# Optimization experiments

Measured on AMD Instinct MI355X. Metric: run time of the kernel, lower is better.

## Reference

```python
import jax, jax.numpy as jnp
import numpy as np

N_NODES = 100000


def _gcn_norm(src, dst, n_nodes, n_edges):
    # PyG gcn_norm with add_self_loops=False: deg over target (col) index
    ones = jnp.ones((n_edges,), dtype=jnp.float32)
    deg = jax.ops.segment_sum(ones, dst, num_segments=n_nodes)
    dinv = jnp.where(deg > 0, jax.lax.rsqrt(deg), 0.0)
    return dinv[src] * dinv[dst]  # [E]


def _arma_conv(x, src, dst, ew, init_w, root_w, bias, n_nodes):
    # x: [N, Fin]; init_w/root_w: [K, Fin, Fout]; bias: [K, 1, Fout]
    h = jnp.einsum('nf,kfo->kno', x, init_w)          # [K, N, Fout]
    msg = h[:, src, :] * ew[None, :, None]             # [K, E, Fout]
    agg = jax.vmap(lambda m: jax.ops.segment_sum(m, dst, num_segments=n_nodes))(msg)
    out = agg + jnp.einsum('nf,kfo->kno', x, root_w) + bias
    return jax.nn.relu(out).mean(axis=0)               # mean over stacks K


def setup_inputs() -> dict:
    key = jax.random.key(0)
    ks = jax.random.split(key, 8)
    n, e = N_NODES, 3200000
    nfeat, hid, nclass, K = 512, 16, 40, 2
    x = jax.random.normal(ks[0], (n, nfeat), dtype=jnp.float32)
    edge_index = jax.random.randint(ks[1], (2, e), 0, n, dtype=jnp.int32)
    s1 = (1.0 / np.sqrt(nfeat)).astype(np.float32) if isinstance(np.sqrt(nfeat), np.ndarray) else np.float32(1.0 / np.sqrt(nfeat))
    s2 = np.float32(1.0 / np.sqrt(hid))
    iw1 = jax.random.normal(ks[2], (K, nfeat, hid), dtype=jnp.float32) * s1
    rw1 = jax.random.normal(ks[3], (K, nfeat, hid), dtype=jnp.float32) * s1
    b1 = jax.random.normal(ks[4], (K, 1, hid), dtype=jnp.float32) * 0.01
    iw2 = jax.random.normal(ks[5], (K, hid, nclass), dtype=jnp.float32) * s2
    rw2 = jax.random.normal(ks[6], (K, hid, nclass), dtype=jnp.float32) * s2
    b2 = jax.random.normal(ks[7], (K, 1, nclass), dtype=jnp.float32) * 0.01
    return {'x': x, 'edge_index': edge_index, 'iw1': iw1, 'rw1': rw1, 'b1': b1,
            'iw2': iw2, 'rw2': rw2, 'b2': b2}


def reference(x, edge_index, iw1, rw1, b1, iw2, rw2, b2):
    src, dst = edge_index[0], edge_index[1]
    n = N_NODES
    ew = _gcn_norm(src, dst, n, src.shape[0])
    h = _arma_conv(x, src, dst, ew, iw1, rw1, b1, n)   # [N, 16]
    out = _arma_conv(h, src, dst, ew, iw2, rw2, b2, n) # [N, nclass]
    return out
```

## Files before the change

kernel.cpp:

```cpp
#include <hip/hip_runtime.h>


#define TB 256
#define CHA 4096

typedef __attribute__((ext_vector_type(8))) short bf8;
typedef __attribute__((ext_vector_type(4))) float f4;

__device__ inline unsigned short f2bf_rne(float f) {
  unsigned int u = __float_as_uint(f);
  unsigned int r = u + 0x7fffu + ((u >> 16) & 1u);
  return (unsigned short)(r >> 16);
}
__device__ inline float bf2f(unsigned short h) {
  return __uint_as_float(((unsigned int)h) << 16);
}
__device__ inline float bflo(unsigned int u) { return __uint_as_float(u << 16); }
__device__ inline float bfhi(unsigned int u) { return __uint_as_float(u & 0xffff0000u); }
__device__ inline unsigned int bfpack(float lo, float hi) {
  return (unsigned int)f2bf_rne(lo) | ((unsigned int)f2bf_rne(hi) << 16);
}

__global__ __launch_bounds__(TB) void k_countA(const int* __restrict__ dst,
                                               int* __restrict__ ccnt, int E) {
  __shared__ int cnt[256];
  int tid = threadIdx.x;
  cnt[tid] = 0;
  __syncthreads();
  int e0 = blockIdx.x * CHA;
  int e1 = min(e0 + CHA, E);
  for (int e = e0 + tid; e < e1; e += TB) atomicAdd(&cnt[dst[e] >> 9], 1);
  __syncthreads();
  if (cnt[tid] > 0) atomicAdd(&ccnt[tid], cnt[tid]);
}

__global__ __launch_bounds__(256) void k_scanC(const int* __restrict__ ccnt,
                                               int* __restrict__ cbase,
                                               int* __restrict__ ccur) {
  __shared__ int sh[256];
  int tid = threadIdx.x;
  int v = ccnt[tid];
  sh[tid] = v;
  __syncthreads();
  for (int d = 1; d < 256; d <<= 1) {
    int t = (tid >= d) ? sh[tid - d] : 0;
    __syncthreads();
    sh[tid] += t;
    __syncthreads();
  }
  int excl = sh[tid] - v;
  cbase[tid] = excl;
  ccur[tid] = excl;
  if (tid == 255) cbase[256] = sh[255];
}

__global__ __launch_bounds__(TB) void k_binA(const int* __restrict__ src,
                                             const int* __restrict__ dst,
                                             int* __restrict__ ccur,
                                             int2* __restrict__ epairs, int E) {
  __shared__ int cnt[256];
  __shared__ int gb[256];
  int tid = threadIdx.x;
  cnt[tid] = 0;
  __syncthreads();
  int e0 = blockIdx.x * CHA;
  int e1 = min(e0 + CHA, E);
  for (int e = e0 + tid; e < e1; e += TB) atomicAdd(&cnt[dst[e] >> 9], 1);
  __syncthreads();
  int c = cnt[tid];
  if (c > 0) gb[tid] = atomicAdd(&ccur[tid], c);
  __syncthreads();
  cnt[tid] = 0;
  __syncthreads();
  for (int e = e0 + tid; e < e1; e += TB) {
    int dv = dst[e];
    int b = dv >> 9;
    int r = atomicAdd(&cnt[b], 1);
    epairs[gb[b] + r] = make_int2(src[e], dv);
  }
}

__global__ __launch_bounds__(TB) void k_binB(const int2* __restrict__ epairs,
                                             const int* __restrict__ cbase,
                                             int* __restrict__ degi,
                                             int* __restrict__ offsets,
                                             int* __restrict__ srcs, int N) {
  __shared__ int cnt[512];
  __shared__ int pre[512];
  int b = blockIdx.x;
  int n0 = b << 9;
  int tid = threadIdx.x;
  int beg = cbase[b], end = cbase[b + 1];
  int i0 = tid, i1 = tid + 256;
  cnt[i0] = 0; cnt[i1] = 0;
  __syncthreads();
  for (int e = beg + tid; e < end; e += TB) atomicAdd(&cnt[epairs[e].y - n0], 1);
  __syncthreads();
  pre[i0] = cnt[i0]; pre[i1] = cnt[i1];
  __syncthreads();
  for (int d = 1; d < 512; d <<= 1) {
    int t0 = (i0 >= d) ? pre[i0 - d] : 0;
    int t1 = (i1 >= d) ? pre[i1 - d] : 0;
    __syncthreads();
    pre[i0] += t0; pre[i1] += t1;
    __syncthreads();
  }
  int e0 = pre[i0] - cnt[i0];
  int e1x = pre[i1] - cnt[i1];
  if (n0 + i0 < N) { degi[n0 + i0] = cnt[i0]; offsets[n0 + i0] = beg + e0; }
  if (n0 + i1 < N) { degi[n0 + i1] = cnt[i1]; offsets[n0 + i1] = beg + e1x; }
  __syncthreads();
  cnt[i0] = e0; cnt[i1] = e1x;
  __syncthreads();
  for (int e = beg + tid; e < end; e += TB) {
    int2 p = epairs[e];
    int pos = atomicAdd(&cnt[p.y - n0], 1);
    srcs[beg + pos] = p.x;
  }
}

__global__ __launch_bounds__(TB) void k_dinv(const int* __restrict__ degi,
                                             float* __restrict__ dinv, int N) {
  int i = blockIdx.x * TB + threadIdx.x;
  if (i < N) {
    int d = degi[i];
    dinv[i] = d > 0 ? rsqrtf((float)d) : 0.0f;
  }
}

__global__ __launch_bounds__(TB) void k_wsplit(const float* __restrict__ iw1,
                                               const float* __restrict__ rw1,
                                               short* __restrict__ Whi,
                                               short* __restrict__ Wlo) {
  int idx = blockIdx.x * TB + threadIdx.x;
  if (idx >= 32768) return;
  int j = idx & 7;
  int l = (idx >> 3) & 63;
  int t = (idx >> 9) & 3;
  int c = idx >> 11;
  int k = c * 32 + (l >> 4) * 8 + j;
  int n = t * 16 + (l & 15);
  float w;
  if (n < 16)
    w = iw1[k * 16 + n];
  else if (n < 32)
    w = iw1[8192 + k * 16 + (n - 16)];
  else if (n < 48)
    w = rw1[k * 16 + (n - 32)];
  else
    w = rw1[8192 + k * 16 + (n - 48)];
  unsigned short h = f2bf_rne(w);
  float res = w - bf2f(h);
  Whi[idx] = (short)h;
  Wlo[idx] = (short)f2bf_rne(res);
}

__global__ __launch_bounds__(TB) void k_gemm1_mfma(const float* __restrict__ x,
                                                   const short* __restrict__ Whi,
                                                   const short* __restrict__ Wlo,
                                                   const float* __restrict__ dinv,
                                                   unsigned short* __restrict__ Hs,
                                                   float* __restrict__ R, int N) {
  int lane = threadIdx.x & 63;
  int wave = threadIdx.x >> 6;
  int row0 = blockIdx.x * 64 + wave * 16;
  int m = lane & 15, quad = lane >> 4;
  int r = row0 + m;
  bool rv = (r < N);
  const float* xr = x + (size_t)r * 512;

  f4 acc[4];
#pragma unroll
  for (int t = 0; t < 4; t++) acc[t] = (f4){0.f, 0.f, 0.f, 0.f};

  for (int c = 0; c < 16; ++c) {
    float xv[8];
    if (rv) {
      f4 a0 = *(const f4*)(xr + c * 32 + quad * 8);
      f4 a1 = *(const f4*)(xr + c * 32 + quad * 8 + 4);
      xv[0] = a0.x; xv[1] = a0.y; xv[2] = a0.z; xv[3] = a0.w;
      xv[4] = a1.x; xv[5] = a1.y; xv[6] = a1.z; xv[7] = a1.w;
    } else {
#pragma unroll
      for (int j = 0; j < 8; ++j) xv[j] = 0.f;
    }
    bf8 ahi, alo;
#pragma unroll
    for (int j = 0; j < 8; ++j) {
      unsigned short h = f2bf_rne(xv[j]);
      float res = xv[j] - bf2f(h);
      ahi[j] = (short)h;
      alo[j] = (short)f2bf_rne(res);
    }
    const short* wb = Whi + ((size_t)(c * 4) * 64 + lane) * 8;
    const short* wl = Wlo + ((size_t)(c * 4) * 64 + lane) * 8;
#pragma unroll
    for (int t = 0; t < 4; ++t) {
      bf8 bh = *(const bf8*)(wb + t * 512);
      bf8 bl = *(const bf8*)(wl + t * 512);
      acc[t] = __builtin_amdgcn_mfma_f32_16x16x32_bf16(ahi, bh, acc[t], 0, 0, 0);
      acc[t] = __builtin_amdgcn_mfma_f32_16x16x32_bf16(alo, bh, acc[t], 0, 0, 0);
      acc[t] = __builtin_amdgcn_mfma_f32_16x16x32_bf16(ahi, bl, acc[t], 0, 0, 0);
    }
  }
  float dv[4];
#pragma unroll
  for (int g = 0; g < 4; ++g) {
    int ro = row0 + quad * 4 + g;
    dv[g] = (ro < N) ? dinv[ro] : 0.f;
  }
#pragma unroll
  for (int t = 0; t < 4; ++t) {
#pragma unroll
    for (int g = 0; g < 4; ++g) {
      int ro = row0 + quad * 4 + g;
      if (ro < N) {
        if (t < 2)
          Hs[(size_t)ro * 32 + t * 16 + m] = f2bf_rne(acc[t][g] * dv[g]);
        else
          R[(size_t)ro * 32 + (t - 2) * 16 + m] = acc[t][g];
      }
    }
  }
}

__global__ __launch_bounds__(TB) void k_prop1(const int* __restrict__ offsets,
                                              const int* __restrict__ degi,
                                              const int* __restrict__ srcs,
                                              const unsigned short* __restrict__ Hs,
                                              const float* __restrict__ R,
                                              const float* __restrict__ dinv,
                                              const float* __restrict__ b1,
                                              float* __restrict__ h,
                                              unsigned short* __restrict__ hs, int N) {
  int tid = blockIdx.x * TB + threadIdx.x;
  int q = tid & 3;
  int n = tid >> 2;
  if (n >= N) return;
  int beg = offsets[n], cnt = degi[n];
  float a[8];
#pragma unroll
  for (int j = 0; j < 8; j++) a[j] = 0.f;
  for (int i = 0; i < cnt; i++) {
    int s = srcs[beg + i];
    uint4 v = *(const uint4*)(Hs + (size_t)s * 32 + q * 8);
    a[0] += bflo(v.x); a[1] += bfhi(v.x);
    a[2] += bflo(v.y); a[3] += bfhi(v.y);
    a[4] += bflo(v.z); a[5] += bfhi(v.z);
    a[6] += bflo(v.w); a[7] += bfhi(v.w);
  }
  float dvn = dinv[n];
  f4 r0 = *(const f4*)(R + (size_t)n * 32 + q * 8);
  f4 r1 = *(const f4*)(R + (size_t)n * 32 + q * 8 + 4);
  float rr[8] = {r0.x, r0.y, r0.z, r0.w, r1.x, r1.y, r1.z, r1.w};
  float vv[8];
#pragma unroll
  for (int j = 0; j < 8; j++) {
    int f = q * 8 + j;
    vv[j] = fmaxf(a[j] * dvn + rr[j] + b1[(f >> 4) * 16 + (f & 15)], 0.f);
  }
  float pv[8];
#pragma unroll
  for (int j = 0; j < 8; j++) pv[j] = __shfl_xor(vv[j], 2);
  if (q < 2) {
    float hv[8];
#pragma unroll
    for (int j = 0; j < 8; j++) hv[j] = 0.5f * (vv[j] + pv[j]);
    f4 o0 = {hv[0], hv[1], hv[2], hv[3]};
    f4 o1 = {hv[4], hv[5], hv[6], hv[7]};
    *(f4*)(h + (size_t)n * 16 + q * 8) = o0;
    *(f4*)(h + (size_t)n * 16 + q * 8 + 4) = o1;
    uint4 ob;
    ob.x = bfpack(hv[0] * dvn, hv[1] * dvn);
    ob.y = bfpack(hv[2] * dvn, hv[3] * dvn);
    ob.z = bfpack(hv[4] * dvn, hv[5] * dvn);
    ob.w = bfpack(hv[6] * dvn, hv[7] * dvn);
    *(uint4*)(hs + (size_t)n * 16 + q * 8) = ob;
  }
}

__global__ __launch_bounds__(TB) void k_prop2(const int* __restrict__ offsets,
                                              const int* __restrict__ degi,
                                              const int* __restrict__ srcs,
                                              const unsigned short* __restrict__ hs,
                                              const float* __restrict__ dinv,
                                              float* __restrict__ Ah, int N) {
  int tid = blockIdx.x * TB + threadIdx.x;
  int q = tid & 3;
  int n = tid >> 2;
  if (n >= N) return;
  int beg = offsets[n], cnt = degi[n];
  float a[4] = {0.f, 0.f, 0.f, 0.f};
  for (int i = 0; i < cnt; i++) {
    int s = srcs[beg + i];
    uint2 v = *(const uint2*)(hs + (size_t)s * 16 + q * 4);
    a[0] += bflo(v.x); a[1] += bfhi(v.x);
    a[2] += bflo(v.y); a[3] += bfhi(v.y);
  }
  float dvn = dinv[n];
  f4 o = {a[0] * dvn, a[1] * dvn, a[2] * dvn, a[3] * dvn};
  *(f4*)(Ah + (size_t)n * 16 + q * 4) = o;
}

__global__ __launch_bounds__(TB) void k_final(const float* __restrict__ Ah,
                                              const float* __restrict__ h,
                                              const float* __restrict__ iw2,
                                              const float* __restrict__ rw2,
                                              const float* __restrict__ b2,
                                              float* __restrict__ out, int N) {
  __shared__ float w_iw[2 * 16 * 40];
  __shared__ float w_rw[2 * 16 * 40];
  __shared__ float w_b[2 * 40];
  for (int i = threadIdx.x; i < 1280; i += TB) {
    w_iw[i] = iw2[i];
    w_rw[i] = rw2[i];
  }
  for (int i = threadIdx.x; i < 80; i += TB) w_b[i] = b2[i];
  __syncthreads();

  int idx = blockIdx.x * TB + threadIdx.x;
  if (idx >= N * 40) return;
  int n = idx / 40;
  int o = idx - n * 40;
  float a[16], hr[16];
#pragma unroll
  for (int f = 0; f < 16; f++) {
    a[f] = Ah[(size_t)n * 16 + f];
    hr[f] = h[(size_t)n * 16 + f];
  }
  float res = 0.f;
#pragma unroll
  for (int k = 0; k < 2; k++) {
    float s = w_b[k * 40 + o];
#pragma unroll
    for (int f = 0; f < 16; f++) {
      s += a[f] * w_iw[(k * 16 + f) * 40 + o];
      s += hr[f] * w_rw[(k * 16 + f) * 40 + o];
    }
    res += fmaxf(s, 0.f);
  }
  out[idx] = 0.5f * res;
}

extern "C" void kernel_launch(void* const* d_in, const int* in_sizes, int n_in,
                              void* d_out, int out_size, void* d_ws, size_t ws_size,
                              hipStream_t stream) {
  const float* x = (const float*)d_in[0];
  const int* ei = (const int*)d_in[1];
  const float* iw1 = (const float*)d_in[2];
  const float* rw1 = (const float*)d_in[3];
  const float* b1 = (const float*)d_in[4];
  const float* iw2 = (const float*)d_in[5];
  const float* rw2 = (const float*)d_in[6];
  const float* b2 = (const float*)d_in[7];
  float* out = (float*)d_out;

  const int N = in_sizes[0] / 512;
  const int E = in_sizes[1] / 2;
  const int* src = ei;
  const int* dst = ei + E;
  const int NC = (N + 511) >> 9;

  char* base = (char*)d_ws;
  size_t off = 0;
  auto alloc = [&](size_t bytes) -> void* {
    off = (off + 255) & ~(size_t)255;
    void* p = base + off;
    off += bytes;
    return p;
  };
  int* degi = (int*)alloc((size_t)N * 4);
  float* dinv = (float*)alloc((size_t)N * 4);
  int* offsets = (int*)alloc((size_t)N * 4);
  int* ccnt = (int*)alloc(260 * 4);
  int* cbase = (int*)alloc(260 * 4);
  int* ccur = (int*)alloc(260 * 4);
  int2* epairs = (int2*)alloc((size_t)E * 8);
  int* srcs = (int*)alloc((size_t)E * 4);
  unsigned short* Hs = (unsigned short*)alloc((size_t)N * 32 * 2);
  float* hbuf = (float*)alloc((size_t)N * 16 * 4);
  unsigned short* hs = (unsigned short*)alloc((size_t)N * 16 * 2);
  float* Ah = (float*)alloc((size_t)N * 16 * 4);
  short* Whi = (short*)alloc(32768 * 2);
  short* Wlo = (short*)alloc(32768 * 2);
  float* R = (float*)epairs;
  (void)ws_size;

  hipMemsetAsync(ccnt, 0, 260 * 4, stream);

  int NBLK = (E + CHA - 1) / CHA;
  k_countA<<<NBLK, TB, 0, stream>>>(dst, ccnt, E);
  k_scanC<<<1, 256, 0, stream>>>(ccnt, cbase, ccur);
  k_binA<<<NBLK, TB, 0, stream>>>(src, dst, ccur, epairs, E);
  k_binB<<<NC, TB, 0, stream>>>(epairs, cbase, degi, offsets, srcs, N);
  k_dinv<<<(N + TB - 1) / TB, TB, 0, stream>>>(degi, dinv, N);
  k_wsplit<<<128, TB, 0, stream>>>(iw1, rw1, Whi, Wlo);
  k_gemm1_mfma<<<(N + 63) / 64, TB, 0, stream>>>(x, Whi, Wlo, dinv, Hs, R, N);
  k_prop1<<<((size_t)N * 4 + TB - 1) / TB, TB, 0, stream>>>(offsets, degi, srcs, Hs, R,
                                                            dinv, b1, hbuf, hs, N);
  k_prop2<<<((size_t)N * 4 + TB - 1) / TB, TB, 0, stream>>>(offsets, degi, srcs, hs,
                                                            dinv, Ah, N);
  k_final<<<((size_t)N * 40 + TB - 1) / TB, TB, 0, stream>>>(Ah, hbuf, iw2, rw2, b2, out, N);
}
```

Before: 604.2 us.

## Replace CSR build with bucketed packed edges and shared-memory atomic aggregation

```diff
diff --git a/kernel.cpp b/kernel.cpp
--- a/kernel.cpp
+++ b/kernel.cpp
@@ -2,6 +2,7 @@
 
 
 #define TB 256
+#define TBP 1024
 #define CHA 4096
 
 typedef __attribute__((ext_vector_type(8))) short bf8;
@@ -12,9 +13,6 @@
   unsigned int r = u + 0x7fffu + ((u >> 16) & 1u);
   return (unsigned short)(r >> 16);
 }
-__device__ inline float bf2f(unsigned short h) {
-  return __uint_as_float(((unsigned int)h) << 16);
-}
 __device__ inline float bflo(unsigned int u) { return __uint_as_float(u << 16); }
 __device__ inline float bfhi(unsigned int u) { return __uint_as_float(u & 0xffff0000u); }
 __device__ inline unsigned int bfpack(float lo, float hi) {
@@ -23,26 +21,27 @@
 
 __global__ __launch_bounds__(TB) void k_countA(const int* __restrict__ dst,
                                                int* __restrict__ ccnt, int E) {
-  __shared__ int cnt[256];
-  int tid = threadIdx.x;
-  cnt[tid] = 0;
+  __shared__ int cnt[512];
+  int tid = threadIdx.x;
+  for (int i = tid; i < 512; i += TB) cnt[i] = 0;
   __syncthreads();
   int e0 = blockIdx.x * CHA;
   int e1 = min(e0 + CHA, E);
-  for (int e = e0 + tid; e < e1; e += TB) atomicAdd(&cnt[dst[e] >> 9], 1);
-  __syncthreads();
-  if (cnt[tid] > 0) atomicAdd(&ccnt[tid], cnt[tid]);
-}
-
-__global__ __launch_bounds__(256) void k_scanC(const int* __restrict__ ccnt,
+  for (int e = e0 + tid; e < e1; e += TB) atomicAdd(&cnt[dst[e] >> 8], 1);
+  __syncthreads();
+  for (int i = tid; i < 512; i += TB)
+    if (cnt[i] > 0) atomicAdd(&ccnt[i], cnt[i]);
+}
+
+__global__ __launch_bounds__(512) void k_scanC(const int* __restrict__ ccnt,
                                                int* __restrict__ cbase,
                                                int* __restrict__ ccur) {
-  __shared__ int sh[256];
+  __shared__ int sh[512];
   int tid = threadIdx.x;
   int v = ccnt[tid];
   sh[tid] = v;
   __syncthreads();
-  for (int d = 1; d < 256; d <<= 1) {
+  for (int d = 1; d < 512; d <<= 1) {
     int t = (tid >= d) ? sh[tid - d] : 0;
     __syncthreads();
     sh[tid] += t;
@@ -51,87 +50,58 @@
   int excl = sh[tid] - v;
   cbase[tid] = excl;
   ccur[tid] = excl;
-  if (tid == 255) cbase[256] = sh[255];
+  if (tid == 511) cbase[512] = sh[511];
 }
 
 __global__ __launch_bounds__(TB) void k_binA(const int* __restrict__ src,
                                              const int* __restrict__ dst,
                                              int* __restrict__ ccur,
-                                             int2* __restrict__ epairs, int E) {
-  __shared__ int cnt[256];
-  __shared__ int gb[256];
-  int tid = threadIdx.x;
-  cnt[tid] = 0;
+                                             unsigned int* __restrict__ epack, int E) {
+  __shared__ int cnt[512];
+  __shared__ int gb[512];
+  int tid = threadIdx.x;
+  for (int i = tid; i < 512; i += TB) cnt[i] = 0;
   __syncthreads();
   int e0 = blockIdx.x * CHA;
   int e1 = min(e0 + CHA, E);
-  for (int e = e0 + tid; e < e1; e += TB) atomicAdd(&cnt[dst[e] >> 9], 1);
-  __syncthreads();
-  int c = cnt[tid];
-  if (c > 0) gb[tid] = atomicAdd(&ccur[tid], c);
-  __syncthreads();
-  cnt[tid] = 0;
+  for (int e = e0 + tid; e < e1; e += TB) atomicAdd(&cnt[dst[e] >> 8], 1);
+  __syncthreads();
+  for (int i = tid; i < 512; i += TB) {
+    int c = cnt[i];
+    if (c > 0) gb[i] = atomicAdd(&ccur[i], c);
+    cnt[i] = 0;
+  }
   __syncthreads();
   for (int e = e0 + tid; e < e1; e += TB) {
     int dv = dst[e];
-    int b = dv >> 9;
+    int b = dv >> 8;
     int r = atomicAdd(&cnt[b], 1);
-    epairs[gb[b] + r] = make_int2(src[e], dv);
-  }
-}
-
-__global__ __launch_bounds__(TB) void k_binB(const int2* __restrict__ epairs,
-                                             const int* __restrict__ cbase,
-                                             int* __restrict__ degi,
-                                             int* __restrict__ offsets,
-                                             int* __restrict__ srcs, int N) {
-  __shared__ int cnt[512];
-  __shared__ int pre[512];
+    epack[gb[b] + r] = ((unsigned int)(dv & 255) << 23) | (unsigned int)src[e];
+  }
+}
+
+__global__ __launch_bounds__(TB) void k_histd(const unsigned int* __restrict__ epack,
+                                              const int* __restrict__ cbase,
+                                              float* __restrict__ dinv, int N) {
+  __shared__ int cnt[256];
   int b = blockIdx.x;
-  int n0 = b << 9;
-  int tid = threadIdx.x;
+  int n0 = b << 8;
+  int tid = threadIdx.x;
+  cnt[tid] = 0;
+  __syncthreads();
   int beg = cbase[b], end = cbase[b + 1];
-  int i0 = tid, i1 = tid + 256;
-  cnt[i0] = 0; cnt[i1] = 0;
-  __syncthreads();
-  for (int e = beg + tid; e < end; e += TB) atomicAdd(&cnt[epairs[e].y - n0], 1);
-  __syncthreads();
-  pre[i0] = cnt[i0]; pre[i1] = cnt[i1];
-  __syncthreads();
-  for (int d = 1; d < 512; d <<= 1) {
-    int t0 = (i0 >= d) ? pre[i0 - d] : 0;
-    int t1 = (i1 >= d) ? pre[i1 - d] : 0;
-    __syncthreads();
-    pre[i0] += t0; pre[i1] += t1;
-    __syncthreads();
-  }
-  int e0 = pre[i0] - cnt[i0];
-  int e1x = pre[i1] - cnt[i1];
-  if (n0 + i0 < N) { degi[n0 + i0] = cnt[i0]; offsets[n0 + i0] = beg + e0; }
-  if (n0 + i1 < N) { degi[n0 + i1] = cnt[i1]; offsets[n0 + i1] = beg + e1x; }
-  __syncthreads();
-  cnt[i0] = e0; cnt[i1] = e1x;
-  __syncthreads();
-  for (int e = beg + tid; e < end; e += TB) {
-    int2 p = epairs[e];
-    int pos = atomicAdd(&cnt[p.y - n0], 1);
-    srcs[beg + pos] = p.x;
-  }
-}
-
-__global__ __launch_bounds__(TB) void k_dinv(const int* __restrict__ degi,
-                                             float* __restrict__ dinv, int N) {
-  int i = blockIdx.x * TB + threadIdx.x;
-  if (i < N) {
-    int d = degi[i];
-    dinv[i] = d > 0 ? rsqrtf((float)d) : 0.0f;
+  for (int e = beg + tid; e < end; e += TB) atomicAdd(&cnt[epack[e] >> 23], 1);
+  __syncthreads();
+  int n = n0 + tid;
+  if (n < N) {
+    int c = cnt[tid];
+    dinv[n] = c > 0 ? rsqrtf((float)c) : 0.f;
   }
 }
 
 __global__ __launch_bounds__(TB) void k_wsplit(const float* __restrict__ iw1,
                                                const float* __restrict__ rw1,
-                                               short* __restrict__ Whi,
-                                               short* __restrict__ Wlo) {
+                                               short* __restrict__ Wt) {
   int idx = blockIdx.x * TB + threadIdx.x;
   if (idx >= 32768) return;
   int j = idx & 7;
@@ -149,15 +119,11 @@
     w = rw1[k * 16 + (n - 32)];
   else
     w = rw1[8192 + k * 16 + (n - 48)];
-  unsigned short h = f2bf_rne(w);
-  float res = w - bf2f(h);
-  Whi[idx] = (short)h;
-  Wlo[idx] = (short)f2bf_rne(res);
+  Wt[idx] = (short)f2bf_rne(w);
 }
 
 __global__ __launch_bounds__(TB) void k_gemm1_mfma(const float* __restrict__ x,
-                                                   const short* __restrict__ Whi,
-                                                   const short* __restrict__ Wlo,
+                                                   const short* __restrict__ Wt,
                                                    const float* __restrict__ dinv,
                                                    unsigned short* __restrict__ Hs,
                                                    float* __restrict__ R, int N) {
@@ -167,40 +133,29 @@
   int m = lane & 15, quad = lane >> 4;
   int r = row0 + m;
   bool rv = (r < N);
-  const float* xr = x + (size_t)r * 512;
+  const unsigned int* xr = (const unsigned int*)(x + (size_t)r * 512);
 
   f4 acc[4];
 #pragma unroll
   for (int t = 0; t < 4; t++) acc[t] = (f4){0.f, 0.f, 0.f, 0.f};
 
   for (int c = 0; c < 16; ++c) {
-    float xv[8];
+    union { unsigned int u[4]; bf8 v; } ah;
     if (rv) {
-      f4 a0 = *(const f4*)(xr + c * 32 + quad * 8);
-      f4 a1 = *(const f4*)(xr + c * 32 + quad * 8 + 4);
-      xv[0] = a0.x; xv[1] = a0.y; xv[2] = a0.z; xv[3] = a0.w;
-      xv[4] = a1.x; xv[5] = a1.y; xv[6] = a1.z; xv[7] = a1.w;
+      uint4 a0 = *(const uint4*)(xr + c * 32 + quad * 8);
+      uint4 a1 = *(const uint4*)(xr + c * 32 + quad * 8 + 4);
+      ah.u[0] = __builtin_amdgcn_perm(a0.y, a0.x, 0x07060302u);
+      ah.u[1] = __builtin_amdgcn_perm(a0.w, a0.z, 0x07060302u);
+      ah.u[2] = __builtin_amdgcn_perm(a1.y, a1.x, 0x07060302u);
+      ah.u[3] = __builtin_amdgcn_perm(a1.w, a1.z, 0x07060302u);
     } else {
-#pragma unroll
-      for (int j = 0; j < 8; ++j) xv[j] = 0.f;
-    }
-    bf8 ahi, alo;
-#pragma unroll
-    for (int j = 0; j < 8; ++j) {
-      unsigned short h = f2bf_rne(xv[j]);
-      float res = xv[j] - bf2f(h);
-      ahi[j] = (short)h;
-      alo[j] = (short)f2bf_rne(res);
-    }
-    const short* wb = Whi + ((size_t)(c * 4) * 64 + lane) * 8;
-    const short* wl = Wlo + ((size_t)(c * 4) * 64 + lane) * 8;
+      ah.u[0] = ah.u[1] = ah.u[2] = ah.u[3] = 0u;
+    }
+    const short* wb = Wt + ((size_t)(c * 4) * 64 + lane) * 8;
 #pragma unroll
     for (int t = 0; t < 4; ++t) {
       bf8 bh = *(const bf8*)(wb + t * 512);
-      bf8 bl = *(const bf8*)(wl + t * 512);
-      acc[t] = __builtin_amdgcn_mfma_f32_16x16x32_bf16(ahi, bh, acc[t], 0, 0, 0);
-      acc[t] = __builtin_amdgcn_mfma_f32_16x16x32_bf16(alo, bh, acc[t], 0, 0, 0);
-      acc[t] = __builtin_amdgcn_mfma_f32_16x16x32_bf16(ahi, bl, acc[t], 0, 0, 0);
+      acc[t] = __builtin_amdgcn_mfma_f32_16x16x32_bf16(ah.v, bh, acc[t], 0, 0, 0);
     }
   }
   float dv[4];
@@ -224,122 +179,119 @@
   }
 }
 
-__global__ __launch_bounds__(TB) void k_prop1(const int* __restrict__ offsets,
-                                              const int* __restrict__ degi,
-                                              const int* __restrict__ srcs,
-                                              const unsigned short* __restrict__ Hs,
-                                              const float* __restrict__ R,
-                                              const float* __restrict__ dinv,
-                                              const float* __restrict__ b1,
-                                              float* __restrict__ h,
-                                              unsigned short* __restrict__ hs, int N) {
-  int tid = blockIdx.x * TB + threadIdx.x;
+__global__ __launch_bounds__(TBP) void k_prop1(const unsigned int* __restrict__ epack,
+                                               const int* __restrict__ cbase,
+                                               const unsigned short* __restrict__ Hs,
+                                               const float* __restrict__ R,
+                                               const float* __restrict__ dinv,
+                                               const float* __restrict__ b1,
+                                               float* __restrict__ h,
+                                               unsigned short* __restrict__ hs, int N) {
+  __shared__ float acc[256 * 33];
+  int b = blockIdx.x;
+  int n0 = b << 8;
+  int tid = threadIdx.x;
+  for (int i = tid; i < 256 * 33; i += TBP) acc[i] = 0.f;
+  __syncthreads();
+  int beg = cbase[b], end = cbase[b + 1];
   int q = tid & 3;
-  int n = tid >> 2;
-  if (n >= N) return;
-  int beg = offsets[n], cnt = degi[n];
-  float a[8];
-#pragma unroll
-  for (int j = 0; j < 8; j++) a[j] = 0.f;
-  for (int i = 0; i < cnt; i++) {
-    int s = srcs[beg + i];
-    uint4 v = *(const uint4*)(Hs + (size_t)s * 32 + q * 8);
-    a[0] += bflo(v.x); a[1] += bfhi(v.x);
-    a[2] += bflo(v.y); a[3] += bfhi(v.y);
-    a[4] += bflo(v.z); a[5] += bfhi(v.z);
-    a[6] += bflo(v.w); a[7] += bfhi(v.w);
-  }
-  float dvn = dinv[n];
-  f4 r0 = *(const f4*)(R + (size_t)n * 32 + q * 8);
-  f4 r1 = *(const f4*)(R + (size_t)n * 32 + q * 8 + 4);
-  float rr[8] = {r0.x, r0.y, r0.z, r0.w, r1.x, r1.y, r1.z, r1.w};
-  float vv[8];
-#pragma unroll
-  for (int j = 0; j < 8; j++) {
-    int f = q * 8 + j;
-    vv[j] = fmaxf(a[j] * dvn + rr[j] + b1[(f >> 4) * 16 + (f & 15)], 0.f);
-  }
-  float pv[8];
-#pragma unroll
-  for (int j = 0; j < 8; j++) pv[j] = __shfl_xor(vv[j], 2);
-  if (q < 2) {
-    float hv[8];
-#pragma unroll
-    for (int j = 0; j < 8; j++) hv[j] = 0.5f * (vv[j] + pv[j]);
-    f4 o0 = {hv[0], hv[1], hv[2], hv[3]};
-    f4 o1 = {hv[4], hv[5], hv[6], hv[7]};
-    *(f4*)(h + (size_t)n * 16 + q * 8) = o0;
-    *(f4*)(h + (size_t)n * 16 + q * 8 + 4) = o1;
-    uint4 ob;
+  for (int e = beg + (tid >> 2); e < end; e += TBP / 4) {
+    unsigned int v = epack[e];
+    int nl = (int)(v >> 23);
+    int s = (int)(v & 0x7FFFFFu);
+    uint4 hv = *(const uint4*)(Hs + (size_t)s * 32 + q * 8);
+    float* a = acc + nl * 33 + q * 8;
+    unsafeAtomicAdd(a + 0, bflo(hv.x)); unsafeAtomicAdd(a + 1, bfhi(hv.x));
+    unsafeAtomicAdd(a + 2, bflo(hv.y)); unsafeAtomicAdd(a + 3, bfhi(hv.y));
+    unsafeAtomicAdd(a + 4, bflo(hv.z)); unsafeAtomicAdd(a + 5, bfhi(hv.z));
+    unsafeAtomicAdd(a + 6, bflo(hv.w)); unsafeAtomicAdd(a + 7, bfhi(hv.w));
+  }
+  __syncthreads();
+  int n = n0 + (tid >> 2);
+  if (n < N) {
+    float dvn = dinv[n];
+    const float* a = acc + (tid >> 2) * 33;
+    f4 r0 = *(const f4*)(R + (size_t)n * 32 + q * 4);
+    f4 r1 = *(const f4*)(R + (size_t)n * 32 + 16 + q * 4);
+    float rr0[4] = {r0.x, r0.y, r0.z, r0.w};
+    float rr1[4] = {r1.x, r1.y, r1.z, r1.w};
+    float hv[4];
+#pragma unroll
+    for (int j = 0; j < 4; j++) {
+      int f = q * 4 + j;
+      float v0 = fmaxf(a[f] * dvn + rr0[j] + b1[f], 0.f);
+      float v1 = fmaxf(a[f + 16] * dvn + rr1[j] + b1[16 + f], 0.f);
+      hv[j] = 0.5f * (v0 + v1);
+    }
+    f4 ho = {hv[0], hv[1], hv[2], hv[3]};
+    *(f4*)(h + (size_t)n * 16 + q * 4) = ho;
+    uint2 ob;
     ob.x = bfpack(hv[0] * dvn, hv[1] * dvn);
     ob.y = bfpack(hv[2] * dvn, hv[3] * dvn);
-    ob.z = bfpack(hv[4] * dvn, hv[5] * dvn);
-    ob.w = bfpack(hv[6] * dvn, hv[7] * dvn);
-    *(uint4*)(hs + (size_t)n * 16 + q * 8) = ob;
-  }
-}
-
-__global__ __launch_bounds__(TB) void k_prop2(const int* __restrict__ offsets,
-                                              const int* __restrict__ degi,
-                                              const int* __restrict__ srcs,
-                                              const unsigned short* __restrict__ hs,
-                                              const float* __restrict__ dinv,
-                                              float* __restrict__ Ah, int N) {
-  int tid = blockIdx.x * TB + threadIdx.x;
+    *(uint2*)(hs + (size_t)n * 16 + q * 4) = ob;
+  }
+}
+
+__global__ __launch_bounds__(TBP) void k_prop2(const unsigned int* __restrict__ epack,
+                                               const int* __restrict__ cbase,
+                                               const unsigned short* __restrict__ hs,
+                                               const float* __restrict__ h,
+                                               const float* __restrict__ dinv,
+                                               const float* __restrict__ iw2,
+                                               const float* __restrict__ rw2,
+                                               const float* __restrict__ b2,
+                                               float* __restrict__ out, int N) {
+  __shared__ float acc[256 * 17];
+  __shared__ float wi[1280];
+  __shared__ float wr[1280];
+  __shared__ float wb[80];
+  int b = blockIdx.x;
+  int n0 = b << 8;
+  int tid = threadIdx.x;
+  for (int i = tid; i < 256 * 17; i += TBP) acc[i] = 0.f;
+  for (int i = tid; i < 1280; i += TBP) { wi[i] = iw2[i]; wr[i] = rw2[i]; }
+  if (tid < 80) wb[tid] = b2[tid];
+  __syncthreads();
+  int beg = cbase[b], end = cbase[b + 1];
   int q = tid & 3;
-  int n = tid >> 2;
-  if (n >= N) return;
-  int beg = offsets[n], cnt = degi[n];
-  float a[4] = {0.f, 0.f, 0.f, 0.f};
-  for (int i = 0; i < cnt; i++) {
-    int s = srcs[beg + i];
-    uint2 v = *(const uint2*)(hs + (size_t)s * 16 + q * 4);
-    a[0] += bflo(v.x); a[1] += bfhi(v.x);
-    a[2] += bflo(v.y); a[3] += bfhi(v.y);
-  }
-  float dvn = dinv[n];
-  f4 o = {a[0] * dvn, a[1] * dvn, a[2] * dvn, a[3] * dvn};
-  *(f4*)(Ah + (size_t)n * 16 + q * 4) = o;
-}
-
-__global__ __launch_bounds__(TB) void k_final(const float* __restrict__ Ah,
-                                              const float* __restrict__ h,
-                                              const float* __restrict__ iw2,
-                                              const float* __restrict__ rw2,
-                                              const float* __restrict__ b2,
-                                              float* __restrict__ out, int N) {
-  __shared__ float w_iw[2 * 16 * 40];
-  __shared__ float w_rw[2 * 16 * 40];
-  __shared__ float w_b[2 * 40];
-  for (int i = threadIdx.x; i < 1280; i += TB) {
-    w_iw[i] = iw2[i];
-    w_rw[i] = rw2[i];
-  }
-  for (int i = threadIdx.x; i < 80; i += TB) w_b[i] = b2[i];
-  __syncthreads();
-
-  int idx = blockIdx.x * TB + threadIdx.x;
-  if (idx >= N * 40) return;
-  int n = idx / 40;
-  int o = idx - n * 40;
-  float a[16], hr[16];
-#pragma unroll
-  for (int f = 0; f < 16; f++) {
-    a[f] = Ah[(size_t)n * 16 + f];
-    hr[f] = h[(size_t)n * 16 + f];
-  }
-  float res = 0.f;
-#pragma unroll
-  for (int k = 0; k < 2; k++) {
-    float s = w_b[k * 40 + o];
-#pragma unroll
-    for (int f = 0; f < 16; f++) {
-      s += a[f] * w_iw[(k * 16 + f) * 40 + o];
-      s += hr[f] * w_rw[(k * 16 + f) * 40 + o];
-    }
-    res += fmaxf(s, 0.f);
-  }
-  out[idx] = 0.5f * res;
+  for (int e = beg + (tid >> 2); e < end; e += TBP / 4) {
+    unsigned int v = epack[e];
+    int nl = (int)(v >> 23);
+    int s = (int)(v & 0x7FFFFFu);
+    uint2 hv = *(const uint2*)(hs + (size_t)s * 16 + q * 4);
+    float* a = acc + nl * 17 + q * 4;
+    unsafeAtomicAdd(a + 0, bflo(hv.x)); unsafeAtomicAdd(a + 1, bfhi(hv.x));
+    unsafeAtomicAdd(a + 2, bflo(hv.y)); unsafeAtomicAdd(a + 3, bfhi(hv.y));
+  }
+  __syncthreads();
+  int n = n0 + (tid >> 2);
+  if (n < N) {
+    float dvn = dinv[n];
+    const float* a = acc + (tid >> 2) * 17;
+    float Ahv[16], hv[16];
+#pragma unroll
+    for (int f = 0; f < 16; f++) Ahv[f] = a[f] * dvn;
+    f4 h0 = *(const f4*)(h + (size_t)n * 16);
+    f4 h1 = *(const f4*)(h + (size_t)n * 16 + 4);
+    f4 h2 = *(const f4*)(h + (size_t)n * 16 + 8);
+    f4 h3 = *(const f4*)(h + (size_t)n * 16 + 12);
+    hv[0] = h0.x; hv[1] = h0.y; hv[2] = h0.z; hv[3] = h0.w;
+    hv[4] = h1.x; hv[5] = h1.y; hv[6] = h1.z; hv[7] = h1.w;
+    hv[8] = h2.x; hv[9] = h2.y; hv[10] = h2.z; hv[11] = h2.w;
+    hv[12] = h3.x; hv[13] = h3.y; hv[14] = h3.z; hv[15] = h3.w;
+    int o0 = q * 10;
+#pragma unroll
+    for (int oi = 0; oi < 10; ++oi) {
+      int o = o0 + oi;
+      float s0 = wb[o], s1 = wb[40 + o];
+#pragma unroll
+      for (int f = 0; f < 16; f++) {
+        s0 += Ahv[f] * wi[f * 40 + o] + hv[f] * wr[f * 40 + o];
+        s1 += Ahv[f] * wi[640 + f * 40 + o] + hv[f] * wr[640 + f * 40 + o];
+      }
+      out[(size_t)n * 40 + o] = 0.5f * (fmaxf(s0, 0.f) + fmaxf(s1, 0.f));
+    }
+  }
 }
 
 extern "C" void kernel_launch(void* const* d_in, const int* in_sizes, int n_in,
@@ -359,7 +311,7 @@
   const int E = in_sizes[1] / 2;
   const int* src = ei;
   const int* dst = ei + E;
-  const int NC = (N + 511) >> 9;
+  const int NC = (N + 255) >> 8;
 
   char* base = (char*)d_ws;
   size_t off = 0;
@@ -369,36 +321,27 @@
     off += bytes;
     return p;
   };
-  int* degi = (int*)alloc((size_t)N * 4);
   float* dinv = (float*)alloc((size_t)N * 4);
-  int* offsets = (int*)alloc((size_t)N * 4);
-  int* ccnt = (int*)alloc(260 * 4);
-  int* cbase = (int*)alloc(260 * 4);
-  int* ccur = (int*)alloc(260 * 4);
-  int2* epairs = (int2*)alloc((size_t)E * 8);
-  int* srcs = (int*)alloc((size_t)E * 4);
+  int* ccnt = (int*)alloc(512 * 4);
+  int* cbase = (int*)alloc(516 * 4);
+  int* ccur = (int*)alloc(512 * 4);
+  unsigned int* epack = (unsigned int*)alloc((size_t)E * 4);
   unsigned short* Hs = (unsigned short*)alloc((size_t)N * 32 * 2);
+  float* R = (float*)alloc((size_t)N * 32 * 4);
   float* hbuf = (float*)alloc((size_t)N * 16 * 4);
   unsigned short* hs = (unsigned short*)alloc((size_t)N * 16 * 2);
-  float* Ah = (float*)alloc((size_t)N * 16 * 4);
-  short* Whi = (short*)alloc(32768 * 2);
-  short* Wlo = (short*)alloc(32768 * 2);
-  float* R = (float*)epairs;
+  short* Wt = (short*)alloc(32768 * 2);
   (void)ws_size;
 
-  hipMemsetAsync(ccnt, 0, 260 * 4, stream);
+  hipMemsetAsync(ccnt, 0, 512 * 4, stream);
 
   int NBLK = (E + CHA - 1) / CHA;
   k_countA<<<NBLK, TB, 0, stream>>>(dst, ccnt, E);
-  k_scanC<<<1, 256, 0, stream>>>(ccnt, cbase, ccur);
-  k_binA<<<NBLK, TB, 0, stream>>>(src, dst, ccur, epairs, E);
-  k_binB<<<NC, TB, 0, stream>>>(epairs, cbase, degi, offsets, srcs, N);
-  k_dinv<<<(N + TB - 1) / TB, TB, 0, stream>>>(degi, dinv, N);
-  k_wsplit<<<128, TB, 0, stream>>>(iw1, rw1, Whi, Wlo);
-  k_gemm1_mfma<<<(N + 63) / 64, TB, 0, stream>>>(x, Whi, Wlo, dinv, Hs, R, N);
-  k_prop1<<<((size_t)N * 4 + TB - 1) / TB, TB, 0, stream>>>(offsets, degi, srcs, Hs, R,
-                                                            dinv, b1, hbuf, hs, N);
-  k_prop2<<<((size_t)N * 4 + TB - 1) / TB, TB, 0, stream>>>(offsets, degi, srcs, hs,
-                                                            dinv, Ah, N);
-  k_final<<<((size_t)N * 40 + TB - 1) / TB, TB, 0, stream>>>(Ah, hbuf, iw2, rw2, b2, out, N);
-}
+  k_scanC<<<1, 512, 0, stream>>>(ccnt, cbase, ccur);
+  k_binA<<<NBLK, TB, 0, stream>>>(src, dst, ccur, epack, E);
+  k_histd<<<NC, TB, 0, stream>>>(epack, cbase, dinv, N);
+  k_wsplit<<<128, TB, 0, stream>>>(iw1, rw1, Wt);
+  k_gemm1_mfma<<<(N + 63) / 64, TB, 0, stream>>>(x, Wt, dinv, Hs, R, N);
+  k_prop1<<<NC, TBP, 0, stream>>>(epack, cbase, Hs, R, dinv, b1, hbuf, hs, N);
+  k_prop2<<<NC, TBP, 0, stream>>>(epack, cbase, hs, hbuf, dinv, iw2, rw2, b2, out, N);
+}
```

After: 1.557 ms. 158% more time.
